# Performance work log

Hardware: AMD Instinct MI355X
Metric: run time of the kernel (lower is better)

The kernel has to match this reference:

```python
import jax, jax.numpy as jnp
import numpy as np

# Experts wrapper (non-distributed path): x is [b, e, n, d]; token slab e is
# routed to expert e. The per-expert Python loop + stack in the original is
# mathematically a grouped (batched-over-experts) MLP, expressed here as
# einsums over the expert axis. Each expert: Linear(d->h), GELU, Linear(h->d).

B, E, N, D, H = 2, 8, 1024, 1024, 4096


def setup_inputs() -> dict:
    key = jax.random.key(0)
    ks = jax.random.split(key, 3)
    x = jax.random.normal(ks[0], (B, E, N, D), dtype=jnp.float32)
    w1 = jax.random.normal(ks[1], (E, D, H), dtype=jnp.float32) * (D ** -0.5)
    b1 = jnp.zeros((E, H), dtype=jnp.float32)
    w2 = jax.random.normal(ks[2], (E, H, D), dtype=jnp.float32) * (H ** -0.5)
    b2 = jnp.zeros((E, D), dtype=jnp.float32)
    return {"x": x, "w1": w1, "b1": b1, "w2": w2, "b2": b2}


def reference(x, w1, b1, w2, b2):
    # x: [b, e, n, d] -> grouped MLP per expert -> [b, e, n, d]
    h = jnp.einsum('bend,edh->benh', x, w1) + b1[None, :, None, :]
    h = jax.nn.gelu(h, approximate=False)  # torch nn.GELU default = exact erf
    out = jnp.einsum('benh,ehd->bend', h, w2) + b2[None, :, None, :]
    return out
```

## Files before the change

### kernel.cpp

```cpp
#include <hip/hip_runtime.h>
#include <stdint.h>

#define B_ 2
#define E_ 8
#define N_ 1024
#define D_ 1024
#define H_ 4096

typedef float f32x4 __attribute__((ext_vector_type(4)));
typedef __bf16 bf16x8 __attribute__((ext_vector_type(8)));
typedef __attribute__((address_space(3))) const unsigned short lds_cus;

__device__ __forceinline__ unsigned short f2bf(float f) {
  union { float f; uint32_t u; } v; v.f = f;
  uint32_t u = v.u;
  return (unsigned short)((u + 0x7FFFu + ((u >> 16) & 1u)) >> 16);
}

__device__ __forceinline__ float gelu_fast(float x) {
  float x3 = x * x * x;
  float y = 0.79788456080286536f * (x + 0.044715f * x3);
  float e = __expf(2.0f * y);
  float t = 1.0f - 2.0f / (e + 1.0f);
  return 0.5f * x * (1.0f + t);
}

__device__ __forceinline__ void gload_lds16(const unsigned short* g, unsigned short* l) {
  __builtin_amdgcn_global_load_lds(
      (__attribute__((address_space(1))) void*)g,
      (__attribute__((address_space(3))) void*)l,
      16, 0, 0);
}

__device__ __forceinline__ bf16x8 lds_read_b128(lds_cus* p) {
  bf16x8 r;
  asm volatile("ds_read_b128 %0, %1" : "=v"(r) : "v"(p));
  return r;
}

__global__ void cvt_x_kernel(const float* __restrict__ in, unsigned short* __restrict__ out, int n4) {
  int idx = blockIdx.x * blockDim.x + threadIdx.x;
  int stride = gridDim.x * blockDim.x;
  const float4* in4 = (const float4*)in;
  ushort4* out4 = (ushort4*)out;
  for (int i = idx; i < n4; i += stride) {
    float4 f = in4[i];
    ushort4 o;
    o.x = f2bf(f.x); o.y = f2bf(f.y); o.z = f2bf(f.z); o.w = f2bf(f.w);
    out4[i] = o;
  }
}

__global__ void transpose_cvt_kernel(const float* __restrict__ in, unsigned short* __restrict__ out,
                                     int R, int C) {
  __shared__ float tile[32][33];
  const size_t eoff = (size_t)blockIdx.z * R * C;
  const float* src = in + eoff;
  unsigned short* dst = out + eoff;
  const int c0 = blockIdx.x * 32, r0 = blockIdx.y * 32;
  const int tx = threadIdx.x, ty = threadIdx.y;
#pragma unroll
  for (int i = 0; i < 4; ++i)
    tile[ty + 8 * i][tx] = src[(size_t)(r0 + ty + 8 * i) * C + c0 + tx];
  __syncthreads();
#pragma unroll
  for (int i = 0; i < 4; ++i)
    dst[(size_t)(c0 + ty + 8 * i) * R + r0 + tx] = f2bf(tile[tx][ty + 8 * i]);
}

template <int K, int NCOLS, bool GELU>
__device__ __forceinline__ void gemm_body(const unsigned short* __restrict__ A,
                                          const unsigned short* __restrict__ Bt,
                                          const float* __restrict__ bias,
                                          unsigned short* __restrict__ OutBf,
                                          float* __restrict__ OutF) {
  constexpr int MT = 2048 / 256;
  constexpr int NTL = NCOLS / 256;
  constexpr int NT = K / 64;

  __shared__ __align__(16) unsigned short A0k0[8192], A0k1[8192], B0k0[8192], B0k1[8192];
  __shared__ __align__(16) unsigned short A1k0[8192], A1k1[8192], B1k0[8192], B1k1[8192];

  const int nwg = gridDim.x;
  const int flat = blockIdx.x;
  const int swz = (flat & 7) * (nwg >> 3) + (flat >> 3);
  const int e = swz / (MT * NTL);
  const int rem = swz - e * (MT * NTL);
  const int nt = rem / MT;
  const int mt = rem - nt * MT;

  const int m0 = mt * 256;
  const int b = m0 >> 10;
  const int nl = m0 & 1023;
  const size_t arow0 = (size_t)((b * E_ + e) * N_ + nl);
  const int n0 = nt * 256;

  const unsigned short* Ab = A + arow0 * K;
  const unsigned short* Bb = Bt + ((size_t)e * NCOLS + n0) * K;

  const int tid = threadIdx.x;
  const int w = tid >> 6;
  const int lane = tid & 63;
  const int wr = w >> 2;
  const int wc = w & 3;
  const int fr = lane & 15;
  const int kg = lane >> 4;
  const int sxor = kg ^ ((lane >> 1) & 3);

  const int scol = (((lane & 3) ^ ((lane >> 3) & 3)) << 3);
  const int srow0 = w * 32 + (lane >> 2);
  const int srow1 = srow0 + 16;
  const unsigned short* aS0 = Ab + (size_t)srow0 * K + scol;
  const unsigned short* aS1 = Ab + (size_t)srow1 * K + scol;
  const unsigned short* bS0 = Bb + (size_t)srow0 * K + scol;
  const unsigned short* bS1 = Bb + (size_t)srow1 * K + scol;

  const int aBase = (wr * 128 + fr) * 32 + sxor * 8;
  const int bBase = (wc * 64 + fr) * 32 + sxor * 8;
  const int rb = kg * 4;

#define STAGE(ARR, S0_, S1_, t, kh) do {                           \
    const size_t ko_ = (size_t)(t) * 64 + (kh) * 32;               \
    gload_lds16(S0_ + ko_, &ARR[w * 1024]);                        \
    gload_lds16(S1_ + ko_, &ARR[w * 1024 + 512]);                  \
  } while (0)

#define WAIT_LGKM() do {                                                      \
    asm volatile("s_waitcnt lgkmcnt(0)");                                     \
    __builtin_amdgcn_sched_barrier(0);                                        \
  } while (0)

#define MFMA_CLUSTER(ROFF)                                                    \
    __builtin_amdgcn_s_setprio(1);                                            \
    _Pragma("unroll")                                                         \
    for (int mi = 0; mi < 4; ++mi)                                            \
      _Pragma("unroll")                                                       \
      for (int ni = 0; ni < 4; ++ni)                                          \
        acc[(ROFF) + mi][ni] =                                                \
            __builtin_amdgcn_mfma_f32_16x16x32_bf16(av[mi], bv[ni],           \
                                                    acc[(ROFF) + mi][ni], 0, 0, 0); \
    __builtin_amdgcn_s_setprio(0);

#define ITER(t, CA0, CA1, CB0, CB1, NA1, NB1) do {                            \
    bf16x8 av[4], bv[4];                                                      \
    _Pragma("unroll")                                                         \
    for (int i = 0; i < 4; ++i) {                                             \
      av[i] = lds_read_b128((lds_cus*)&CA0[aBase + i * 512]);                 \
      bv[i] = lds_read_b128((lds_cus*)&CB0[bBase + i * 512]);                 \
    }                                                                         \
    if ((t) + 1 < NT) STAGE(NA1, aS0, aS1, (t) + 1, 1);                       \
    __builtin_amdgcn_s_barrier();                                             \
    WAIT_LGKM();                                                              \
    MFMA_CLUSTER(0)                                                           \
    __builtin_amdgcn_s_barrier();                                             \
    _Pragma("unroll")                                                         \
    for (int i = 0; i < 4; ++i)                                               \
      av[i] = lds_read_b128((lds_cus*)&CA0[aBase + 2048 + i * 512]);          \
    if ((t) + 1 < NT) STAGE(NB1, bS0, bS1, (t) + 1, 1);                       \
    __builtin_amdgcn_s_barrier();                                             \
    WAIT_LGKM();                                                              \
    MFMA_CLUSTER(4)                                                           \
    __builtin_amdgcn_s_barrier();                                             \
    _Pragma("unroll")                                                         \
    for (int i = 0; i < 4; ++i) {                                             \
      av[i] = lds_read_b128((lds_cus*)&CA1[aBase + i * 512]);                 \
      bv[i] = lds_read_b128((lds_cus*)&CB1[bBase + i * 512]);                 \
    }                                                                         \
    if ((t) + 2 < NT) STAGE(CA0, aS0, aS1, (t) + 2, 0);                       \
    __builtin_amdgcn_s_barrier();                                             \
    WAIT_LGKM();                                                              \
    MFMA_CLUSTER(0)                                                           \
    __builtin_amdgcn_s_barrier();                                             \
    _Pragma("unroll")                                                         \
    for (int i = 0; i < 4; ++i)                                               \
      av[i] = lds_read_b128((lds_cus*)&CA1[aBase + 2048 + i * 512]);          \
    if ((t) + 2 < NT) STAGE(CB0, bS0, bS1, (t) + 2, 0);                       \
    __builtin_amdgcn_s_barrier();                                             \
    WAIT_LGKM();                                                              \
    MFMA_CLUSTER(4)                                                           \
    if ((t) + 2 < NT) { asm volatile("s_waitcnt vmcnt(4)" ::: "memory"); }    \
    else              { asm volatile("s_waitcnt vmcnt(0)" ::: "memory"); }    \
    __builtin_amdgcn_s_barrier();                                             \
  } while (0)

  f32x4 acc[8][4];
#pragma unroll
  for (int i = 0; i < 8; ++i)
#pragma unroll
    for (int j = 0; j < 4; ++j)
      acc[i][j] = (f32x4){0.f, 0.f, 0.f, 0.f};

  STAGE(A0k0, aS0, aS1, 0, 0); STAGE(B0k0, bS0, bS1, 0, 0);
  STAGE(A0k1, aS0, aS1, 0, 1); STAGE(B0k1, bS0, bS1, 0, 1);
  STAGE(A1k0, aS0, aS1, 1, 0); STAGE(B1k0, bS0, bS1, 1, 0);
  asm volatile("s_waitcnt vmcnt(4)" ::: "memory");
  __builtin_amdgcn_s_barrier();

#pragma unroll 1
  for (int tt = 0; tt < NT; tt += 2) {
    ITER(tt,     A0k0, A0k1, B0k0, B0k1, A1k1, B1k1);
    ITER(tt + 1, A1k0, A1k1, B1k0, B1k1, A0k1, B0k1);
  }

#undef ITER
#undef MFMA_CLUSTER
#undef WAIT_LGKM
#undef STAGE

  if constexpr (GELU) {
    float bval[4];
#pragma unroll
    for (int ni = 0; ni < 4; ++ni)
      bval[ni] = bias[(size_t)e * NCOLS + n0 + wc * 64 + ni * 16 + fr];
    const size_t gcb = (size_t)n0 + wc * 64 + fr;
#pragma unroll
    for (int MI = 0; MI < 8; ++MI) {
#pragma unroll
      for (int j = 0; j < 4; ++j) {
        const size_t orow = arow0 + (size_t)(wr * 128 + MI * 16 + rb + j);
        unsigned short* rp = OutBf + orow * NCOLS + gcb;
#pragma unroll
        for (int ni = 0; ni < 4; ++ni)
          __builtin_nontemporal_store(f2bf(gelu_fast(acc[MI][ni][j] + bval[ni])),
                                      &rp[ni * 16]);
      }
    }
  } else {
#pragma unroll
    for (int ni = 0; ni < 4; ++ni) {
      const int gc = n0 + wc * 64 + ni * 16 + fr;
      const float bval = bias[(size_t)e * NCOLS + gc];
#pragma unroll
      for (int MI = 0; MI < 8; ++MI) {
        const size_t orow = arow0 + (size_t)(wr * 128 + MI * 16 + rb);
#pragma unroll
        for (int j = 0; j < 4; ++j)
          __builtin_nontemporal_store(acc[MI][ni][j] + bval,
                                      &OutF[(orow + j) * NCOLS + gc]);
      }
    }
  }
}

__global__ __launch_bounds__(512, 2)
void gemm_mlp1(const unsigned short* __restrict__ A, const unsigned short* __restrict__ Bt,
               const float* __restrict__ bias, unsigned short* __restrict__ OutBf) {
  gemm_body<D_, H_, true>(A, Bt, bias, OutBf, nullptr);
}

__global__ __launch_bounds__(512, 2)
void gemm_mlp2(const unsigned short* __restrict__ A, const unsigned short* __restrict__ Bt,
               const float* __restrict__ bias, float* __restrict__ OutF) {
  gemm_body<H_, D_, false>(A, Bt, bias, nullptr, OutF);
}

extern "C" void kernel_launch(void* const* d_in, const int* in_sizes, int n_in,
                              void* d_out, int out_size, void* d_ws, size_t ws_size,
                              hipStream_t stream) {
  const float* x  = (const float*)d_in[0];
  const float* w1 = (const float*)d_in[1];
  const float* b1 = (const float*)d_in[2];
  const float* w2 = (const float*)d_in[3];
  const float* b2 = (const float*)d_in[4];
  float* out = (float*)d_out;

  const size_t xN  = (size_t)B_ * E_ * N_ * D_;
  const size_t w1N = (size_t)E_ * D_ * H_;
  const size_t w2N = (size_t)E_ * H_ * D_;
  const size_t hN  = (size_t)B_ * E_ * N_ * H_;
  const size_t needed = (xN + w1N + w2N + hN) * 2;
  if (ws_size < needed) return;

  unsigned short* xb  = (unsigned short*)d_ws;
  unsigned short* w1t = xb + xN;
  unsigned short* w2t = w1t + w1N;
  unsigned short* hb  = w2t + w2N;

  dim3 tb(32, 8);
  transpose_cvt_kernel<<<dim3(D_ / 32, H_ / 32, E_), tb, 0, stream>>>(w2, w2t, H_, D_);
  transpose_cvt_kernel<<<dim3(H_ / 32, D_ / 32, E_), tb, 0, stream>>>(w1, w1t, D_, H_);
  cvt_x_kernel<<<2048, 256, 0, stream>>>(x, xb, (int)(xN / 4));

  gemm_mlp1<<<E_ * 8 * (H_ / 256), 512, 0, stream>>>(xb, w1t, b1, hb);
  gemm_mlp2<<<E_ * 8 * (D_ / 256), 512, 0, stream>>>(hb, w2t, b2, out);
}
```

Baseline: 434.0 us.

## Split first GEMM into separate 128x128-tile kernel with simple single-buffered loop

The first GEMM (x·W1 with GELU) becomes its own kernel using 128x128 tiles, 256 threads, 4 workgroups per CU, and a single-buffered LDS loop with direct global-to-LDS loads and an XOR swizzle. The second GEMM keeps the 256x256 double-buffered pipeline, now specialised. Nontemporal stores are replaced with plain stores in both epilogues. The intent is more resident workgroups and a simpler schedule for the short-K first GEMM, at the cost of lower per-tile reuse and no explicit prefetch overlap within each workgroup.

```diff
diff --git a/kernel.cpp b/kernel.cpp
--- a/kernel.cpp
+++ b/kernel.cpp
@@ -68,15 +68,128 @@
     dst[(size_t)(c0 + ty + 8 * i) * R + r0 + tx] = f2bf(tile[tx][ty + 8 * i]);
 }
 
-template <int K, int NCOLS, bool GELU>
-__device__ __forceinline__ void gemm_body(const unsigned short* __restrict__ A,
-                                          const unsigned short* __restrict__ Bt,
-                                          const float* __restrict__ bias,
-                                          unsigned short* __restrict__ OutBf,
-                                          float* __restrict__ OutF) {
-  constexpr int MT = 2048 / 256;
-  constexpr int NTL = NCOLS / 256;
+__global__ __launch_bounds__(256, 4)
+void gemm_mlp1(const unsigned short* __restrict__ A,
+               const unsigned short* __restrict__ Bt,
+               const float* __restrict__ bias,
+               unsigned short* __restrict__ Out) {
+  constexpr int K = D_;
+  constexpr int NCOLS = H_;
   constexpr int NT = K / 64;
+  constexpr int MT = 16;
+  constexpr int NTL = 32;
+
+  __shared__ __align__(16) unsigned short Alds[8192];
+  __shared__ __align__(16) unsigned short Blds[8192];
+
+  const int nwg = gridDim.x;
+  const int flat = blockIdx.x;
+  const int swz = (flat & 7) * (nwg >> 3) + (flat >> 3);
+  const int e = swz / (MT * NTL);
+  const int rem = swz - e * (MT * NTL);
+  const int nt = rem >> 4;
+  const int mt = rem & 15;
+
+  const int m0 = mt * 128;
+  const int b = m0 >> 10;
+  const int nl = m0 & 1023;
+  const size_t arow0 = (size_t)((b * E_ + e) * N_ + nl);
+  const int n0 = nt * 128;
+
+  const int tid = threadIdx.x;
+  const int wid = tid >> 6;
+  const int lane = tid & 63;
+  const int wr = wid >> 1, wc = wid & 1;
+  const int fr = lane & 15;
+  const int kg = lane >> 4;
+
+  const int lr = lane >> 3;
+  const int sl = lane & 7;
+  const unsigned short* aSrc[4];
+  const unsigned short* bSrc[4];
+  unsigned short* aDst[4];
+  unsigned short* bDst[4];
+#pragma unroll
+  for (int j = 0; j < 4; ++j) {
+    const int c = wid * 4 + j;
+    const int grow = c * 8 + lr;
+    const int f = (grow >> 1) & 7;
+    const int ksl = (sl ^ f) << 3;
+    aSrc[j] = A + (arow0 + grow) * K + ksl;
+    bSrc[j] = Bt + ((size_t)e * NCOLS + n0 + grow) * K + ksl;
+    aDst[j] = &Alds[c * 512];
+    bDst[j] = &Blds[c * 512];
+  }
+
+  const int f_r = (fr >> 1) & 7;
+  const int slot0 = kg ^ f_r;
+  const int aRow = (wr * 64 + fr) * 64;
+  const int bRow = (wc * 64 + fr) * 64;
+  const int rb = kg * 4;
+
+  f32x4 acc[4][4];
+#pragma unroll
+  for (int i = 0; i < 4; ++i)
+#pragma unroll
+    for (int j = 0; j < 4; ++j)
+      acc[i][j] = (f32x4){0.f, 0.f, 0.f, 0.f};
+
+#pragma unroll 1
+  for (int t = 0; t < NT; ++t) {
+    __syncthreads();
+#pragma unroll
+    for (int j = 0; j < 4; ++j) {
+      gload_lds16(aSrc[j] + t * 64, aDst[j]);
+      gload_lds16(bSrc[j] + t * 64, bDst[j]);
+    }
+    __syncthreads();
+#pragma unroll
+    for (int kh = 0; kh < 2; ++kh) {
+      const int sx = (slot0 ^ (kh << 2)) << 3;
+      bf16x8 av[4], bv[4];
+#pragma unroll
+      for (int i = 0; i < 4; ++i) {
+        av[i] = *(const bf16x8*)&Alds[aRow + i * 1024 + sx];
+        bv[i] = *(const bf16x8*)&Blds[bRow + i * 1024 + sx];
+      }
+      __builtin_amdgcn_s_setprio(1);
+#pragma unroll
+      for (int mi = 0; mi < 4; ++mi)
+#pragma unroll
+        for (int ni = 0; ni < 4; ++ni)
+          acc[mi][ni] = __builtin_amdgcn_mfma_f32_16x16x32_bf16(av[mi], bv[ni], acc[mi][ni], 0, 0, 0);
+      __builtin_amdgcn_s_setprio(0);
+    }
+  }
+
+  float bval[4];
+#pragma unroll
+  for (int ni = 0; ni < 4; ++ni)
+    bval[ni] = bias[(size_t)e * NCOLS + n0 + wc * 64 + ni * 16 + fr];
+  const size_t gcb = (size_t)n0 + wc * 64 + fr;
+#pragma unroll
+  for (int mi = 0; mi < 4; ++mi) {
+#pragma unroll
+    for (int j = 0; j < 4; ++j) {
+      const size_t orow = arow0 + (size_t)(wr * 64 + mi * 16 + rb + j);
+      unsigned short* rp = Out + orow * NCOLS + gcb;
+#pragma unroll
+      for (int ni = 0; ni < 4; ++ni)
+        rp[ni * 16] = f2bf(gelu_fast(acc[mi][ni][j] + bval[ni]));
+    }
+  }
+}
+
+__global__ __launch_bounds__(512, 2)
+void gemm_mlp2(const unsigned short* __restrict__ A,
+               const unsigned short* __restrict__ Bt,
+               const float* __restrict__ bias,
+               float* __restrict__ OutF) {
+  constexpr int K = H_;
+  constexpr int NCOLS = D_;
+  constexpr int NT = K / 64;
+  constexpr int MT = 8;
+  constexpr int NTL = 4;
 
   __shared__ __align__(16) unsigned short A0k0[8192], A0k1[8192], B0k0[8192], B0k1[8192];
   __shared__ __align__(16) unsigned short A1k0[8192], A1k1[8192], B1k0[8192], B1k1[8192];
@@ -207,51 +320,18 @@
 #undef WAIT_LGKM
 #undef STAGE
 
-  if constexpr (GELU) {
-    float bval[4];
-#pragma unroll
-    for (int ni = 0; ni < 4; ++ni)
-      bval[ni] = bias[(size_t)e * NCOLS + n0 + wc * 64 + ni * 16 + fr];
-    const size_t gcb = (size_t)n0 + wc * 64 + fr;
+#pragma unroll
+  for (int ni = 0; ni < 4; ++ni) {
+    const int gc = n0 + wc * 64 + ni * 16 + fr;
+    const float bval = bias[(size_t)e * NCOLS + gc];
 #pragma unroll
     for (int MI = 0; MI < 8; ++MI) {
-#pragma unroll
-      for (int j = 0; j < 4; ++j) {
-        const size_t orow = arow0 + (size_t)(wr * 128 + MI * 16 + rb + j);
-        unsigned short* rp = OutBf + orow * NCOLS + gcb;
-#pragma unroll
-        for (int ni = 0; ni < 4; ++ni)
-          __builtin_nontemporal_store(f2bf(gelu_fast(acc[MI][ni][j] + bval[ni])),
-                                      &rp[ni * 16]);
-      }
+      const size_t orow = arow0 + (size_t)(wr * 128 + MI * 16 + rb);
+#pragma unroll
+      for (int j = 0; j < 4; ++j)
+        OutF[(orow + j) * NCOLS + gc] = acc[MI][ni][j] + bval;
     }
-  } else {
-#pragma unroll
-    for (int ni = 0; ni < 4; ++ni) {
-      const int gc = n0 + wc * 64 + ni * 16 + fr;
-      const float bval = bias[(size_t)e * NCOLS + gc];
-#pragma unroll
-      for (int MI = 0; MI < 8; ++MI) {
-        const size_t orow = arow0 + (size_t)(wr * 128 + MI * 16 + rb);
-#pragma unroll
-        for (int j = 0; j < 4; ++j)
-          __builtin_nontemporal_store(acc[MI][ni][j] + bval,
-                                      &OutF[(orow + j) * NCOLS + gc]);
-      }
-    }
-  }
-}
-
-__global__ __launch_bounds__(512, 2)
-void gemm_mlp1(const unsigned short* __restrict__ A, const unsigned short* __restrict__ Bt,
-               const float* __restrict__ bias, unsigned short* __restrict__ OutBf) {
-  gemm_body<D_, H_, true>(A, Bt, bias, OutBf, nullptr);
-}
-
-__global__ __launch_bounds__(512, 2)
-void gemm_mlp2(const unsigned short* __restrict__ A, const unsigned short* __restrict__ Bt,
-               const float* __restrict__ bias, float* __restrict__ OutF) {
-  gemm_body<H_, D_, false>(A, Bt, bias, nullptr, OutF);
+  }
 }
 
 extern "C" void kernel_launch(void* const* d_in, const int* in_sizes, int n_in,
@@ -281,6 +361,6 @@
   transpose_cvt_kernel<<<dim3(H_ / 32, D_ / 32, E_), tb, 0, stream>>>(w1, w1t, D_, H_);
   cvt_x_kernel<<<2048, 256, 0, stream>>>(x, xb, (int)(xN / 4));
 
-  gemm_mlp1<<<E_ * 8 * (H_ / 256), 512, 0, stream>>>(xb, w1t, b1, hb);
+  gemm_mlp1<<<E_ * 16 * 32, 256, 0, stream>>>(xb, w1t, b1, hb);
   gemm_mlp2<<<E_ * 8 * (D_ / 256), 512, 0, stream>>>(hb, w2t, b2, out);
 }
```

Result: faster. 425.1 us (-2.0%).
